# Kernel tuning notes

Hardware: AMD Instinct MI355X
Metric: run time of the kernel (lower is better)

Reference implementation:

```python
import jax, jax.numpy as jnp
import numpy as np

EPS = 1e-5


def setup_inputs() -> dict:
    key = jax.random.key(0)
    ks = jax.random.split(key, 4)
    B, C, H, W = 8, 256, 32, 32
    heads, head_dim = 8, 32
    attn_dim = heads * head_dim  # 256
    x = jax.random.normal(ks[0], (B, C, H, W), dtype=jnp.float32)
    gamma = jnp.ones((C,), dtype=jnp.float32)
    beta = jnp.zeros((C,), dtype=jnp.float32)
    w_qkv = jax.random.normal(ks[1], (3 * attn_dim, C), dtype=jnp.float32) * 0.02
    b_qkv = jnp.zeros((3 * attn_dim,), dtype=jnp.float32)
    w_proj = jax.random.normal(ks[2], (C, attn_dim), dtype=jnp.float32) * 0.02
    b_proj = jnp.zeros((C,), dtype=jnp.float32)
    return {"x": x, "gamma": gamma, "beta": beta, "w_qkv": w_qkv,
            "b_qkv": b_qkv, "w_proj": w_proj, "b_proj": b_proj}


def reference(x, gamma, beta, w_qkv, b_qkv, w_proj, b_proj):
    B, C, H, W = x.shape
    heads, head_dim = 8, 32
    scale = head_dim ** -0.5
    N = H * W

    # per-pixel LayerNorm over the channel axis (channels-first)
    mu = jnp.mean(x, axis=1, keepdims=True)
    var = jnp.var(x, axis=1, keepdims=True)
    xn = (x - mu) * jax.lax.rsqrt(var + EPS)
    xn = xn * gamma[None, :, None, None] + beta[None, :, None, None]

    # 1x1 conv QKV == channel matmul: [B, 3*attn_dim, H, W]
    qkv = jnp.einsum('oc,bchw->bohw', w_qkv, xn) + b_qkv[None, :, None, None]
    qkv = qkv.reshape(B, heads, 3 * head_dim, N)
    q, k, v = jnp.split(qkv, 3, axis=2)  # each [B, heads, head_dim, N]

    # attn[b,h,n,m] = sum_d q[b,h,d,n] * k[b,h,d,m]
    attn = jnp.einsum('bhdn,bhdm->bhnm', q, k) * scale
    attn = jax.nn.softmax(attn, axis=-1)

    # out[b,h,d,n] = sum_m v[b,h,d,m] * attn[b,h,n,m]
    out = jnp.einsum('bhdm,bhnm->bhdn', v, attn)
    out = out.reshape(B, heads * head_dim, H, W)

    out = jnp.einsum('oc,bchw->bohw', w_proj, out) + b_proj[None, :, None, None]
    return x + out
```

## Files before the change

kernel.cpp:

```cpp
#include <hip/hip_runtime.h>
#include <hip/hip_bf16.h>

#define BB 8
#define CC 256
#define NPIX 1024
#define NH 8
#define HD 32
#define QKVO 768
#define EPS 1e-5f

typedef __attribute__((ext_vector_type(4)))  float floatx4;
typedef __attribute__((ext_vector_type(16))) float floatx16;
typedef __attribute__((ext_vector_type(8)))  short bf16x8;


__global__ __launch_bounds__(256) void w_prep(const float* __restrict__ wq,
                                              const float* __restrict__ wp,
                                              __hip_bfloat16* __restrict__ wqf,
                                              __hip_bfloat16* __restrict__ wpf) {
    int idx = blockIdx.x * 256 + threadIdx.x;
    const float* src;
    __hip_bfloat16* dst;
    int n;
    if (idx < 24576) { src = wq; dst = wqf; n = idx; }
    else             { src = wp; dst = wpf; n = idx - 24576; }
    const int lane = n & 63, kks = (n >> 6) & 7, tile = n >> 9;
    const int row = tile * 16 + (lane & 15);
    const int col = kks * 32 + (lane >> 4) * 8;
    const float* s = src + (size_t)row * CC + col;
    union { bf16x8 v; __hip_bfloat16 h[8]; } pk;
    #pragma unroll
    for (int j = 0; j < 8; ++j) pk.h[j] = __float2bfloat16(s[j]);
    *(bf16x8*)(dst + (size_t)n * 8) = pk.v;
}

__global__ __launch_bounds__(512) void ln_qkv(const float* __restrict__ x,
                                              const float* __restrict__ gamma,
                                              const float* __restrict__ beta,
                                              const __hip_bfloat16* __restrict__ wqf,
                                              const float* __restrict__ bq,
                                              __hip_bfloat16* __restrict__ qf,
                                              __hip_bfloat16* __restrict__ kf,
                                              __hip_bfloat16* __restrict__ vf) {
    __shared__ short xbn[16 * 256];
    __shared__ float s_part[32][17];
    __shared__ float q_part[32][17];
    __shared__ float s_mu[16], s_rs[16];

    const int tid  = threadIdx.x;
    const int P0   = blockIdx.x * 16;
    const int b    = P0 >> 10;
    const int nloc = tid & 15;
    const int g    = tid >> 4;
    const float* xb = x + (size_t)b * CC * NPIX + (P0 & 1023);

    float vals[8];
    float s = 0.f, s2 = 0.f;
    #pragma unroll
    for (int j = 0; j < 8; ++j) {
        float v = xb[(size_t)(g * 8 + j) * NPIX + nloc];
        vals[j] = v; s += v; s2 += v * v;
    }
    s_part[g][nloc] = s; q_part[g][nloc] = s2;
    __syncthreads();
    if (tid < 16) {
        float ss = 0.f, qq = 0.f;
        #pragma unroll
        for (int k = 0; k < 32; ++k) { ss += s_part[k][tid]; qq += q_part[k][tid]; }
        float mu  = ss * (1.f / CC);
        float var = qq * (1.f / CC) - mu * mu;
        s_mu[tid] = mu; s_rs[tid] = rsqrtf(var + EPS);
    }
    __syncthreads();

    {
        const float mu = s_mu[nloc], rs = s_rs[nloc];
        union { bf16x8 v; unsigned short us[8]; } pk;
        #pragma unroll
        for (int j = 0; j < 8; ++j) {
            int c = g * 8 + j;
            pk.us[j] = __bfloat16_as_ushort(__float2bfloat16((vals[j] - mu) * rs * gamma[c] + beta[c]));
        }
        int idx = (nloc * 256 + g * 8) ^ (nloc << 3);
        *(bf16x8*)(&xbn[idx]) = pk.v;
    }
    __syncthreads();

    const int w = tid >> 6, lane = tid & 63, lr = lane & 15, lg = lane >> 4;
    const int otb = w * 6;
    floatx4 acc[6] = {};
    for (int kks = 0; kks < 8; ++kks) {
        const int aidx = (lr * 256 + kks * 32 + lg * 8) ^ (lr << 3);
        bf16x8 a = *(const bf16x8*)(&xbn[aidx]);
        #pragma unroll
        for (int nt = 0; nt < 6; ++nt) {
            bf16x8 bfr = *(const bf16x8*)(wqf + (((size_t)(otb + nt) * 8 + kks) * 64 + lane) * 8);
            acc[nt] = __builtin_amdgcn_mfma_f32_16x16x32_bf16(a, bfr, acc[nt], 0, 0, 0);
        }
    }
    const float QSCALE = 0.25503495f;
    const int mb32   = (P0 & 16) + lg * 4;
    const int tile32 = (P0 & 1023) >> 5;
    #pragma unroll
    for (int nt = 0; nt < 6; ++nt) {
        const int o = (otb + nt) * 16 + lr;
        const int h = o / 96, om = o % 96;
        const float bias = bq[o];
        const size_t fb = (size_t)((b * NH + h) * 32 + tile32) * 1024;
        if (om < 64) {
            const int d = om & 31;
            const bool isq = (om < 32);
            __hip_bfloat16* dst = (isq ? qf : kf);
            const float sc = isq ? QSCALE : 1.0f;
            const int off = (d >> 4) * 512 + ((d >> 3) & 1) * 256 + (d & 7);
            #pragma unroll
            for (int r = 0; r < 4; ++r)
                dst[fb + off + (size_t)(mb32 + r) * 8] = __float2bfloat16((acc[nt][r] + bias) * sc);
        } else {
            const int d = om - 64;
            const int half = mb32 >> 4, hi2 = (mb32 >> 3) & 1, j0 = mb32 & 7;
            union { unsigned short us[4]; uint2 u; } pv;
            #pragma unroll
            for (int r = 0; r < 4; ++r)
                pv.us[r] = __bfloat16_as_ushort(__float2bfloat16(acc[nt][r] + bias));
            *(uint2*)(vf + fb + half * 512 + (d + 32 * hi2) * 8 + j0) = pv.u;
        }
    }
}

__global__ __launch_bounds__(1024, 8) void attn_fused8(const __hip_bfloat16* __restrict__ qf,
                                                       const __hip_bfloat16* __restrict__ kf,
                                                       const __hip_bfloat16* __restrict__ vf,
                                                       __hip_bfloat16* __restrict__ obf) {
    __shared__ float smem_f[3 * 4 * 64 * 17];
    float (*m_lds)[4][64][17] = (float (*)[4][64][17]) smem_f;
    float (*t_lds)[32][33]    = (float (*)[32][33])    smem_f;

    const int flat = blockIdx.y * 64 + blockIdx.x;
    const int bh   = (flat & 7) * 8 + ((flat >> 3) & 7);
    const int qg   = flat >> 6;
    const int b = bh >> 3, h = bh & 7;
    const int tid = threadIdx.x, w = tid >> 6, lane = tid & 63;
    const int lc = lane & 31, hi = lane >> 5;
    const int kq = w >> 2;
    const int qt = w & 3;
    const int n_tile = qg * 4 + qt;

    const __hip_bfloat16* qb = qf + (size_t)(bh * 32 + n_tile) * 1024;
    bf16x8 q0 = *(const bf16x8*)(qb + lane * 8);
    bf16x8 q1 = *(const bf16x8*)(qb + 512 + lane * 8);

    const __hip_bfloat16* kb = kf + (size_t)(bh * 32 + kq * 8) * 1024 + lane * 8;
    const __hip_bfloat16* vb = vf + (size_t)(bh * 32 + kq * 8) * 1024 + lane * 8;

    floatx16 oacc = {0.f,0.f,0.f,0.f,0.f,0.f,0.f,0.f,0.f,0.f,0.f,0.f,0.f,0.f,0.f,0.f};
    float ls0 = 0.f, ls1 = 0.f, ls2 = 0.f, ls3 = 0.f;

    #pragma unroll 2
    for (int t = 0; t < 8; ++t) {
        bf16x8 k0 = *(const bf16x8*)(kb + t * 1024);
        bf16x8 k1 = *(const bf16x8*)(kb + t * 1024 + 512);
        bf16x8 v0 = *(const bf16x8*)(vb + t * 1024);
        bf16x8 v1 = *(const bf16x8*)(vb + t * 1024 + 512);

        floatx16 st = {0.f,0.f,0.f,0.f,0.f,0.f,0.f,0.f,0.f,0.f,0.f,0.f,0.f,0.f,0.f,0.f};
        __builtin_amdgcn_s_setprio(1);
        st = __builtin_amdgcn_mfma_f32_32x32x16_bf16(k0, q0, st, 0, 0, 0);
        st = __builtin_amdgcn_mfma_f32_32x32x16_bf16(k1, q1, st, 0, 0, 0);
        __builtin_amdgcn_s_setprio(0);
        float p[16];
        #pragma unroll
        for (int r = 0; r < 16; ++r) p[r] = __builtin_amdgcn_exp2f(st[r]);
        ls0 += p[0] + p[4] + p[8]  + p[12];
        ls1 += p[1] + p[5] + p[9]  + p[13];
        ls2 += p[2] + p[6] + p[10] + p[14];
        ls3 += p[3] + p[7] + p[11] + p[15];
        unsigned int wpk[8];
        #pragma unroll
        for (int k2 = 0; k2 < 8; ++k2)
            asm("v_cvt_pk_bf16_f32 %0, %1, %2" : "=v"(wpk[k2]) : "v"(p[2*k2]), "v"(p[2*k2+1]));
        asm("v_permlane32_swap_b32 %0, %1" : "+v"(wpk[0]), "+v"(wpk[2]));
        asm("v_permlane32_swap_b32 %0, %1" : "+v"(wpk[1]), "+v"(wpk[3]));
        asm("v_permlane32_swap_b32 %0, %1" : "+v"(wpk[4]), "+v"(wpk[6]));
        asm("v_permlane32_swap_b32 %0, %1" : "+v"(wpk[5]), "+v"(wpk[7]));
        union { bf16x8 v; unsigned int u[4]; } pb0, pb1;
        pb0.u[0] = wpk[0]; pb0.u[1] = wpk[1]; pb0.u[2] = wpk[2]; pb0.u[3] = wpk[3];
        pb1.u[0] = wpk[4]; pb1.u[1] = wpk[5]; pb1.u[2] = wpk[6]; pb1.u[3] = wpk[7];
        __builtin_amdgcn_s_setprio(1);
        oacc = __builtin_amdgcn_mfma_f32_32x32x16_bf16(v0, pb0.v, oacc, 0, 0, 0);
        oacc = __builtin_amdgcn_mfma_f32_32x32x16_bf16(v1, pb1.v, oacc, 0, 0, 0);
        __builtin_amdgcn_s_setprio(0);
    }
    float lsum = (ls0 + ls1) + (ls2 + ls3);

    if (kq > 0) {
        #pragma unroll
        for (int r = 0; r < 16; ++r) m_lds[kq - 1][qt][lane][r] = oacc[r];
        m_lds[kq - 1][qt][lane][16] = lsum;
    }
    __syncthreads();
    float inv = 0.f;
    if (kq == 0) {
        #pragma unroll
        for (int s = 0; s < 3; ++s) {
            #pragma unroll
            for (int r = 0; r < 16; ++r) oacc[r] += m_lds[s][qt][lane][r];
            lsum += m_lds[s][qt][lane][16];
        }
        lsum += __shfl_xor(lsum, 32);
        inv = 1.0f / lsum;
    }
    __syncthreads();
    if (kq == 0) {
        #pragma unroll
        for (int r = 0; r < 16; ++r) {
            int d = (r & 3) + 8 * (r >> 2) + 4 * hi;
            t_lds[qt][lc][d] = oacc[r] * inv;
        }
    }
    __syncthreads();
    if (kq == 0) {
        const int q = lane >> 4, nl = lane & 15;
        #pragma unroll
        for (int half = 0; half < 2; ++half) {
            union { __hip_bfloat16 h16[8]; uint4 u4; } ov;
            #pragma unroll
            for (int j = 0; j < 8; ++j)
                ov.h16[j] = __float2bfloat16(t_lds[qt][half * 16 + nl][q * 8 + j]);
            *(uint4*)(obf + (((size_t)(b * 64 + n_tile * 2 + half) * 8 + h) * 64 + lane) * 8) = ov.u4;
        }
    }
}

__global__ __launch_bounds__(256) void gemm_proj_res(const __hip_bfloat16* __restrict__ obf,
                                                     const __hip_bfloat16* __restrict__ wpf,
                                                     const float* __restrict__ bp,
                                                     const float* __restrict__ x,
                                                     float* __restrict__ out) {
    const int c0 = blockIdx.x * 64, n0 = blockIdx.y * 64, b = blockIdx.z;
    const int tid = threadIdx.x, w = tid >> 6, lane = tid & 63;
    const int lr = lane & 15, lg = lane >> 4;
    const int ct = (c0 >> 4) + w;
    const int nt16 = n0 >> 4;

    floatx4 acc[4] = {};
    for (int kks = 0; kks < 8; ++kks) {
        bf16x8 aa = *(const bf16x8*)(wpf + (((size_t)ct * 8 + kks) * 64 + lane) * 8);
        #pragma unroll
        for (int nt = 0; nt < 4; ++nt) {
            bf16x8 bfr = *(const bf16x8*)(obf + (((size_t)(b * 64 + nt16 + nt) * 8 + kks) * 64 + lane) * 8);
            acc[nt] = __builtin_amdgcn_mfma_f32_16x16x32_bf16(aa, bfr, acc[nt], 0, 0, 0);
        }
    }
    #pragma unroll
    for (int nt = 0; nt < 4; ++nt)
        #pragma unroll
        for (int r = 0; r < 4; ++r) {
            int c = c0 + w * 16 + lg * 4 + r;
            int n = n0 + nt * 16 + lr;
            size_t idx = ((size_t)b * CC + c) * NPIX + n;
            out[idx] = acc[nt][r] + bp[c] + x[idx];
        }
}

extern "C" void kernel_launch(void* const* d_in, const int* in_sizes, int n_in,
                              void* d_out, int out_size, void* d_ws, size_t ws_size,
                              hipStream_t stream) {
    const float* x      = (const float*)d_in[0];
    const float* gamma  = (const float*)d_in[1];
    const float* beta   = (const float*)d_in[2];
    const float* w_qkv  = (const float*)d_in[3];
    const float* b_qkv  = (const float*)d_in[4];
    const float* w_proj = (const float*)d_in[5];
    const float* b_proj = (const float*)d_in[6];
    float* out = (float*)d_out;

    char* ws = (char*)d_ws;
    __hip_bfloat16* qfb  = (__hip_bfloat16*)(ws);
    __hip_bfloat16* kfb  = (__hip_bfloat16*)(ws + (4  << 20));
    __hip_bfloat16* vfb  = (__hip_bfloat16*)(ws + (8  << 20));
    __hip_bfloat16* obf  = (__hip_bfloat16*)(ws + (12 << 20));
    __hip_bfloat16* wqf  = (__hip_bfloat16*)(ws + (16 << 20));
    __hip_bfloat16* wpf  = (__hip_bfloat16*)(ws + (16 << 20) + (512 << 10));

    w_prep<<<128, 256, 0, stream>>>(w_qkv, w_proj, wqf, wpf);
    ln_qkv<<<BB * NPIX / 16, 512, 0, stream>>>(x, gamma, beta, wqf, b_qkv, qfb, kfb, vfb);
    attn_fused8<<<dim3(64, 8), 1024, 0, stream>>>(qfb, kfb, vfb, obf);
    gemm_proj_res<<<dim3(CC / 64, NPIX / 64, BB), 256, 0, stream>>>(obf, wpf, b_proj, x, out);
}
```

Baseline: 48.99 us.

## Fuse attention with output projection and residual into one kernel

The attention kernel is rebuilt so each block handles one batch and one 32-query tile across all 8 heads. Two waves per head split the key range in halves, the normalized output is staged in LDS as bf16, and the projection GEMM plus bias and residual run in the same block. This removes the obf round trip through global memory and one kernel launch. In exchange the grid shrinks from 512 to 256 blocks, and each wave does twice as many key iterations, so there is less parallelism and less key-split.

```diff
diff --git a/kernel.cpp b/kernel.cpp
--- a/kernel.cpp
+++ b/kernel.cpp
@@ -72,7 +72,6 @@
         s_mu[tid] = mu; s_rs[tid] = rsqrtf(var + EPS);
     }
     __syncthreads();
-
     {
         const float mu = s_mu[nloc], rs = s_rs[nloc];
         union { bf16x8 v; unsigned short us[8]; } pk;
@@ -128,36 +127,39 @@
     }
 }
 
-__global__ __launch_bounds__(1024, 8) void attn_fused8(const __hip_bfloat16* __restrict__ qf,
-                                                       const __hip_bfloat16* __restrict__ kf,
-                                                       const __hip_bfloat16* __restrict__ vf,
-                                                       __hip_bfloat16* __restrict__ obf) {
-    __shared__ float smem_f[3 * 4 * 64 * 17];
-    float (*m_lds)[4][64][17] = (float (*)[4][64][17]) smem_f;
-    float (*t_lds)[32][33]    = (float (*)[32][33])    smem_f;
-
-    const int flat = blockIdx.y * 64 + blockIdx.x;
-    const int bh   = (flat & 7) * 8 + ((flat >> 3) & 7);
-    const int qg   = flat >> 6;
-    const int b = bh >> 3, h = bh & 7;
+__global__ __launch_bounds__(1024, 8) void attn_proj(const __hip_bfloat16* __restrict__ qf,
+                                                     const __hip_bfloat16* __restrict__ kf,
+                                                     const __hip_bfloat16* __restrict__ vf,
+                                                     const __hip_bfloat16* __restrict__ wpf,
+                                                     const float* __restrict__ bp,
+                                                     const float* __restrict__ x,
+                                                     float* __restrict__ out) {
+    __shared__ __align__(16) char smem_raw[34816 + 16384];
+    float (*m_lds)[64][17] = (float (*)[64][17]) smem_raw;
+    __hip_bfloat16* o_lds  = (__hip_bfloat16*)(smem_raw + 34816);
+
+    const int bid = blockIdx.x;
+    const int b   = bid & 7;
+    const int t32 = bid >> 3;
     const int tid = threadIdx.x, w = tid >> 6, lane = tid & 63;
+    const int lr = lane & 15, lg = lane >> 4;
     const int lc = lane & 31, hi = lane >> 5;
-    const int kq = w >> 2;
-    const int qt = w & 3;
-    const int n_tile = qg * 4 + qt;
-
-    const __hip_bfloat16* qb = qf + (size_t)(bh * 32 + n_tile) * 1024;
+    const int h  = w >> 1;
+    const int mh = w & 1;
+    const int bh = b * NH + h;
+
+    const __hip_bfloat16* qb = qf + (size_t)(bh * 32 + t32) * 1024;
     bf16x8 q0 = *(const bf16x8*)(qb + lane * 8);
     bf16x8 q1 = *(const bf16x8*)(qb + 512 + lane * 8);
 
-    const __hip_bfloat16* kb = kf + (size_t)(bh * 32 + kq * 8) * 1024 + lane * 8;
-    const __hip_bfloat16* vb = vf + (size_t)(bh * 32 + kq * 8) * 1024 + lane * 8;
+    const __hip_bfloat16* kb = kf + (size_t)(bh * 32 + mh * 16) * 1024 + lane * 8;
+    const __hip_bfloat16* vb = vf + (size_t)(bh * 32 + mh * 16) * 1024 + lane * 8;
 
     floatx16 oacc = {0.f,0.f,0.f,0.f,0.f,0.f,0.f,0.f,0.f,0.f,0.f,0.f,0.f,0.f,0.f,0.f};
     float ls0 = 0.f, ls1 = 0.f, ls2 = 0.f, ls3 = 0.f;
 
     #pragma unroll 2
-    for (int t = 0; t < 8; ++t) {
+    for (int t = 0; t < 16; ++t) {
         bf16x8 k0 = *(const bf16x8*)(kb + t * 1024);
         bf16x8 k1 = *(const bf16x8*)(kb + t * 1024 + 512);
         bf16x8 v0 = *(const bf16x8*)(vb + t * 1024);
@@ -193,74 +195,61 @@
     }
     float lsum = (ls0 + ls1) + (ls2 + ls3);
 
-    if (kq > 0) {
-        #pragma unroll
-        for (int r = 0; r < 16; ++r) m_lds[kq - 1][qt][lane][r] = oacc[r];
-        m_lds[kq - 1][qt][lane][16] = lsum;
-    }
-    __syncthreads();
-    float inv = 0.f;
-    if (kq == 0) {
-        #pragma unroll
-        for (int s = 0; s < 3; ++s) {
-            #pragma unroll
-            for (int r = 0; r < 16; ++r) oacc[r] += m_lds[s][qt][lane][r];
-            lsum += m_lds[s][qt][lane][16];
-        }
+    if (mh == 1) {
+        #pragma unroll
+        for (int r = 0; r < 16; ++r) m_lds[h][lane][r] = oacc[r];
+        m_lds[h][lane][16] = lsum;
+    }
+    __syncthreads();
+    if (mh == 0) {
+        #pragma unroll
+        for (int r = 0; r < 16; ++r) oacc[r] += m_lds[h][lane][r];
+        lsum += m_lds[h][lane][16];
         lsum += __shfl_xor(lsum, 32);
-        inv = 1.0f / lsum;
-    }
-    __syncthreads();
-    if (kq == 0) {
+        float inv = 1.0f / lsum;
+        float (*ts)[33] = (float (*)[33]) &m_lds[h][0][0];
         #pragma unroll
         for (int r = 0; r < 16; ++r) {
             int d = (r & 3) + 8 * (r >> 2) + 4 * hi;
-            t_lds[qt][lc][d] = oacc[r] * inv;
-        }
-    }
-    __syncthreads();
-    if (kq == 0) {
+            ts[lc][d] = oacc[r] * inv;
+        }
+    }
+    __syncthreads();
+    if (mh == 0) {
+        float (*ts)[33] = (float (*)[33]) &m_lds[h][0][0];
         const int q = lane >> 4, nl = lane & 15;
         #pragma unroll
-        for (int half = 0; half < 2; ++half) {
+        for (int nt = 0; nt < 2; ++nt) {
             union { __hip_bfloat16 h16[8]; uint4 u4; } ov;
             #pragma unroll
             for (int j = 0; j < 8; ++j)
-                ov.h16[j] = __float2bfloat16(t_lds[qt][half * 16 + nl][q * 8 + j]);
-            *(uint4*)(obf + (((size_t)(b * 64 + n_tile * 2 + half) * 8 + h) * 64 + lane) * 8) = ov.u4;
-        }
-    }
-}
-
-__global__ __launch_bounds__(256) void gemm_proj_res(const __hip_bfloat16* __restrict__ obf,
-                                                     const __hip_bfloat16* __restrict__ wpf,
-                                                     const float* __restrict__ bp,
-                                                     const float* __restrict__ x,
-                                                     float* __restrict__ out) {
-    const int c0 = blockIdx.x * 64, n0 = blockIdx.y * 64, b = blockIdx.z;
-    const int tid = threadIdx.x, w = tid >> 6, lane = tid & 63;
-    const int lr = lane & 15, lg = lane >> 4;
-    const int ct = (c0 >> 4) + w;
-    const int nt16 = n0 >> 4;
-
-    floatx4 acc[4] = {};
-    for (int kks = 0; kks < 8; ++kks) {
-        bf16x8 aa = *(const bf16x8*)(wpf + (((size_t)ct * 8 + kks) * 64 + lane) * 8);
-        #pragma unroll
-        for (int nt = 0; nt < 4; ++nt) {
-            bf16x8 bfr = *(const bf16x8*)(obf + (((size_t)(b * 64 + nt16 + nt) * 8 + kks) * 64 + lane) * 8);
-            acc[nt] = __builtin_amdgcn_mfma_f32_16x16x32_bf16(aa, bfr, acc[nt], 0, 0, 0);
-        }
-    }
-    #pragma unroll
-    for (int nt = 0; nt < 4; ++nt)
-        #pragma unroll
-        for (int r = 0; r < 4; ++r) {
-            int c = c0 + w * 16 + lg * 4 + r;
-            int n = n0 + nt * 16 + lr;
-            size_t idx = ((size_t)b * CC + c) * NPIX + n;
-            out[idx] = acc[nt][r] + bp[c] + x[idx];
-        }
+                ov.h16[j] = __float2bfloat16(ts[nt * 16 + nl][q * 8 + j]);
+            *(uint4*)(o_lds + (((size_t)nt * 8 + h) * 64 + lane) * 8) = ov.u4;
+        }
+    }
+    __syncthreads();
+
+    {
+        const int ct = w;
+        floatx4 acc2[2] = {};
+        for (int kks = 0; kks < 8; ++kks) {
+            bf16x8 aa = *(const bf16x8*)(wpf + (((size_t)ct * 8 + kks) * 64 + lane) * 8);
+            #pragma unroll
+            for (int nt = 0; nt < 2; ++nt) {
+                bf16x8 bb = *(const bf16x8*)(o_lds + (((size_t)nt * 8 + kks) * 64 + lane) * 8);
+                acc2[nt] = __builtin_amdgcn_mfma_f32_16x16x32_bf16(aa, bb, acc2[nt], 0, 0, 0);
+            }
+        }
+        #pragma unroll
+        for (int nt = 0; nt < 2; ++nt)
+            #pragma unroll
+            for (int r = 0; r < 4; ++r) {
+                int c = ct * 16 + lg * 4 + r;
+                int n = t32 * 32 + nt * 16 + lr;
+                size_t idx = ((size_t)b * CC + c) * NPIX + n;
+                out[idx] = acc2[nt][r] + bp[c] + x[idx];
+            }
+    }
 }
 
 extern "C" void kernel_launch(void* const* d_in, const int* in_sizes, int n_in,
@@ -279,12 +268,10 @@
     __hip_bfloat16* qfb  = (__hip_bfloat16*)(ws);
     __hip_bfloat16* kfb  = (__hip_bfloat16*)(ws + (4  << 20));
     __hip_bfloat16* vfb  = (__hip_bfloat16*)(ws + (8  << 20));
-    __hip_bfloat16* obf  = (__hip_bfloat16*)(ws + (12 << 20));
-    __hip_bfloat16* wqf  = (__hip_bfloat16*)(ws + (16 << 20));
-    __hip_bfloat16* wpf  = (__hip_bfloat16*)(ws + (16 << 20) + (512 << 10));
+    __hip_bfloat16* wqf  = (__hip_bfloat16*)(ws + (12 << 20));
+    __hip_bfloat16* wpf  = (__hip_bfloat16*)(ws + (12 << 20) + (512 << 10));
 
     w_prep<<<128, 256, 0, stream>>>(w_qkv, w_proj, wqf, wpf);
     ln_qkv<<<BB * NPIX / 16, 512, 0, stream>>>(x, gamma, beta, wqf, b_qkv, qfb, kfb, vfb);
-    attn_fused8<<<dim3(64, 8), 1024, 0, stream>>>(qfb, kfb, vfb, obf);
-    gemm_proj_res<<<dim3(CC / 64, NPIX / 64, BB), 256, 0, stream>>>(obf, wpf, b_proj, x, out);
-}
+    attn_proj<<<BB * 32, 1024, 0, stream>>>(qfb, kfb, vfb, wpf, b_proj, x, out);
+}
```

Result: faster. 46.76 us (-4.6%).
